# Kernel tuning notes

Hardware: AMD Instinct MI355X
Metric: run time of the kernel (lower is better)

## Reference

```python
import jax, jax.numpy as jnp
import numpy as np

N_NODES = 1_000_000
N_EDGES = 16_000_000
F_IN, F_H1, F_H2, N_CLS = 32, 16, 8, 5
N_GRAPHS = 10_000


def setup_inputs() -> dict:
    key = jax.random.key(0)
    ks = jax.random.split(key, 10)
    x = jax.random.normal(ks[0], (N_NODES, F_IN), dtype=jnp.float32)
    edge_index = jax.random.randint(ks[1], (2, N_EDGES), 0, N_NODES, dtype=jnp.int32)
    batch = jnp.sort(jax.random.randint(ks[2], (N_NODES,), 0, N_GRAPHS, dtype=jnp.int32))
    # learned params (Glorot-ish scale)
    W1 = jax.random.normal(ks[3], (F_IN, F_H1), dtype=jnp.float32) / np.sqrt(F_IN)
    b1 = jnp.zeros((F_H1,), dtype=jnp.float32)
    W2 = jax.random.normal(ks[4], (F_H1, F_H2), dtype=jnp.float32) / np.sqrt(F_H1)
    b2 = jnp.zeros((F_H2,), dtype=jnp.float32)
    Wl = jax.random.normal(ks[5], (F_H2, N_CLS), dtype=jnp.float32) / np.sqrt(F_H2)
    bl = jnp.zeros((N_CLS,), dtype=jnp.float32)
    return {"x": x, "edge_index": edge_index, "batch": batch, "num_graphs": N_GRAPHS,
            "W1": W1, "b1": b1, "W2": W2, "b2": b2, "Wl": Wl, "bl": bl}


def _gcn_conv(x, W, b, src, dst, deg_inv_sqrt, norm_e, num_nodes):
    # h = X W, then symmetric-normalized aggregation with self loops:
    # out_i = sum_{(j->i)} norm_ji * h_j + deg_i^{-1} * h_i + b
    h = x @ W                                  # [N, F_out]
    msg = h[src] * norm_e[:, None]             # [E, F_out] gather + scale
    agg = jax.ops.segment_sum(msg, dst, num_segments=num_nodes)
    self_loop = h * (deg_inv_sqrt * deg_inv_sqrt)[:, None]
    return agg + self_loop + b


def reference(x, edge_index, batch, num_graphs, W1, b1, W2, b2, Wl, bl):
    num_nodes = x.shape[0]
    src, dst = edge_index[0], edge_index[1]
    # degrees including self loops (GCN: A_hat = A + I)
    deg = jax.ops.segment_sum(jnp.ones_like(dst, dtype=x.dtype), dst,
                              num_segments=num_nodes) + 1.0
    deg_inv_sqrt = jax.lax.rsqrt(deg)
    norm_e = deg_inv_sqrt[src] * deg_inv_sqrt[dst]   # [E]

    h = _gcn_conv(x, W1, b1, src, dst, deg_inv_sqrt, norm_e, num_nodes)
    h = jax.nn.relu(h)
    h = _gcn_conv(h, W2, b2, src, dst, deg_inv_sqrt, norm_e, num_nodes)
    h = jax.nn.relu(h)

    # global_mean_pool over graph ids
    sums = jax.ops.segment_sum(h, batch, num_segments=num_graphs)     # [G, F_H2]
    cnts = jax.ops.segment_sum(jnp.ones((num_nodes,), dtype=h.dtype), batch,
                               num_segments=num_graphs)
    pooled = sums / jnp.maximum(cnts, 1.0)[:, None]
    return pooled @ Wl + bl
```

## Files before the change

kernel.cpp:

```cpp
#include <hip/hip_runtime.h>


namespace {

constexpr int F_IN = 32, F_H1 = 16, F_H2 = 8, N_CLS = 5;

__global__ void k_deg(const int* __restrict__ dst, float* __restrict__ deg, int E) {
  int e = blockIdx.x * blockDim.x + threadIdx.x;
  if (e < E) atomicAdd(&deg[dst[e]], 1.0f);
}

__global__ void k_dis(float* __restrict__ d, int N) {
  int i = blockIdx.x * blockDim.x + threadIdx.x;
  if (i < N) d[i] = rsqrtf(d[i] + 1.0f);
}

__global__ void k_mm1(const float* __restrict__ x, const float* __restrict__ W,
                      float* __restrict__ h, int N) {
  __shared__ float w[F_IN * F_H1];
  for (int k = threadIdx.x; k < F_IN * F_H1; k += blockDim.x) w[k] = W[k];
  __syncthreads();
  int i = blockIdx.x * blockDim.x + threadIdx.x;
  if (i >= N) return;
  const float4* xr = reinterpret_cast<const float4*>(x + (size_t)i * F_IN);
  float acc[F_H1];
#pragma unroll
  for (int f = 0; f < F_H1; ++f) acc[f] = 0.f;
#pragma unroll
  for (int k4 = 0; k4 < F_IN / 4; ++k4) {
    float4 v = xr[k4];
    float vv[4] = {v.x, v.y, v.z, v.w};
#pragma unroll
    for (int j = 0; j < 4; ++j) {
      const float* wr = &w[(k4 * 4 + j) * F_H1];
#pragma unroll
      for (int f = 0; f < F_H1; ++f) acc[f] = fmaf(vv[j], wr[f], acc[f]);
    }
  }
  float4* hr = reinterpret_cast<float4*>(h + (size_t)i * F_H1);
#pragma unroll
  for (int q = 0; q < F_H1 / 4; ++q)
    hr[q] = make_float4(acc[q * 4], acc[q * 4 + 1], acc[q * 4 + 2], acc[q * 4 + 3]);
}

__global__ void k_mm2(const float* __restrict__ in, const float* __restrict__ W,
                      float* __restrict__ h, int N) {
  __shared__ float w[F_H1 * F_H2];
  for (int k = threadIdx.x; k < F_H1 * F_H2; k += blockDim.x) w[k] = W[k];
  __syncthreads();
  int i = blockIdx.x * blockDim.x + threadIdx.x;
  if (i >= N) return;
  const float4* xr = reinterpret_cast<const float4*>(in + (size_t)i * F_H1);
  float acc[F_H2];
#pragma unroll
  for (int f = 0; f < F_H2; ++f) acc[f] = 0.f;
#pragma unroll
  for (int k4 = 0; k4 < F_H1 / 4; ++k4) {
    float4 v = xr[k4];
    float vv[4] = {v.x, v.y, v.z, v.w};
#pragma unroll
    for (int j = 0; j < 4; ++j) {
      const float* wr = &w[(k4 * 4 + j) * F_H2];
#pragma unroll
      for (int f = 0; f < F_H2; ++f) acc[f] = fmaf(vv[j], wr[f], acc[f]);
    }
  }
  float4* hr = reinterpret_cast<float4*>(h + (size_t)i * F_H2);
#pragma unroll
  for (int q = 0; q < F_H2 / 4; ++q)
    hr[q] = make_float4(acc[q * 4], acc[q * 4 + 1], acc[q * 4 + 2], acc[q * 4 + 3]);
}

template <int F>
__global__ void k_edge(const int* __restrict__ src, const int* __restrict__ dst,
                       const float* __restrict__ dis, const float* __restrict__ h,
                       float* __restrict__ agg, int total) {
  int gid = blockIdx.x * blockDim.x + threadIdx.x;
  if (gid >= total) return;
  int e = gid / F, f = gid % F;
  int s = src[e], d = dst[e];
  float nw = dis[s] * dis[d];
  atomicAdd(&agg[d * F + f], h[s * F + f] * nw);
}

template <int F>
__global__ void k_combine(const float* __restrict__ h, const float* __restrict__ dis,
                          const float* __restrict__ b, float* __restrict__ agg,
                          int total) {
  int gid = blockIdx.x * blockDim.x + threadIdx.x;
  if (gid >= total) return;
  int i = gid / F, f = gid % F;
  float di = dis[i];
  float v = agg[gid] + h[gid] * di * di + b[f];
  agg[gid] = fmaxf(v, 0.f);
}

__global__ void k_combine_pool(const float* __restrict__ h2, const float* __restrict__ agg2,
                               const float* __restrict__ dis, const float* __restrict__ b,
                               const int* __restrict__ batch, float* __restrict__ pooled,
                               float* __restrict__ cnts, int total) {
  int gid = blockIdx.x * blockDim.x + threadIdx.x;
  if (gid >= total) return;
  int i = gid >> 3, f = gid & 7;
  float di = dis[i];
  float v = fmaxf(agg2[gid] + h2[gid] * di * di + b[f], 0.f);
  int g = batch[i];
  atomicAdd(&pooled[g * F_H2 + f], v);
  if (f == 0) atomicAdd(&cnts[g], 1.0f);
}

__global__ void k_final(const float* __restrict__ pooled, const float* __restrict__ cnts,
                        const float* __restrict__ Wl, const float* __restrict__ bl,
                        float* __restrict__ out, int total) {
  int gid = blockIdx.x * blockDim.x + threadIdx.x;
  if (gid >= total) return;
  int g = gid / N_CLS, c = gid % N_CLS;
  float s = 0.f;
#pragma unroll
  for (int f = 0; f < F_H2; ++f) s += pooled[g * F_H2 + f] * Wl[f * N_CLS + c];
  out[gid] = s / fmaxf(cnts[g], 1.f) + bl[c];
}

}

extern "C" void kernel_launch(void* const* d_in, const int* in_sizes, int n_in,
                              void* d_out, int out_size, void* d_ws, size_t ws_size,
                              hipStream_t stream) {
  const float* x   = (const float*)d_in[0];
  const int* ei    = (const int*)d_in[1];
  const int* batch = (const int*)d_in[2];
  const float* W1 = (const float*)d_in[4];
  const float* b1 = (const float*)d_in[5];
  const float* W2 = (const float*)d_in[6];
  const float* b2 = (const float*)d_in[7];
  const float* Wl = (const float*)d_in[8];
  const float* bl = (const float*)d_in[9];

  const int N = in_sizes[0] / F_IN;
  const int E = in_sizes[1] / 2;
  const int G = out_size / N_CLS;
  const int* src = ei;
  const int* dstp = ei + E;

  float* ws = (float*)d_ws;
  float* dis    = ws;
  float* A      = ws + N;
  float* B      = A + (size_t)N * F_H1;
  float* h2     = A;
  float* agg2   = A + (size_t)N * F_H2;
  float* pooled = B + (size_t)N * F_H1;
  float* cnts   = pooled + (size_t)G * F_H2;

  const int BLK = 256;

  hipMemsetAsync(dis, 0, (size_t)N * sizeof(float), stream);
  hipMemsetAsync(B, 0, (size_t)N * F_H1 * sizeof(float), stream);
  hipMemsetAsync(pooled, 0, ((size_t)G * F_H2 + G) * sizeof(float), stream);

  k_deg<<<(E + BLK - 1) / BLK, BLK, 0, stream>>>(dstp, dis, E);
  k_dis<<<(N + BLK - 1) / BLK, BLK, 0, stream>>>(dis, N);

  k_mm1<<<(N + BLK - 1) / BLK, BLK, 0, stream>>>(x, W1, A, N);
  {
    int total = E * F_H1;
    k_edge<F_H1><<<(unsigned)((long long)(total + BLK - 1) / BLK), BLK, 0, stream>>>(
        src, dstp, dis, A, B, total);
  }
  k_combine<F_H1><<<(N * F_H1 + BLK - 1) / BLK, BLK, 0, stream>>>(A, dis, b1, B, N * F_H1);

  hipMemsetAsync(agg2, 0, (size_t)N * F_H2 * sizeof(float), stream);
  k_mm2<<<(N + BLK - 1) / BLK, BLK, 0, stream>>>(B, W2, h2, N);
  {
    int total = E * F_H2;
    k_edge<F_H2><<<(unsigned)((long long)(total + BLK - 1) / BLK), BLK, 0, stream>>>(
        src, dstp, dis, h2, agg2, total);
  }
  k_combine_pool<<<(N * F_H2 + BLK - 1) / BLK, BLK, 0, stream>>>(
      h2, agg2, dis, b2, batch, pooled, cnts, N * F_H2);

  k_final<<<(G * N_CLS + BLK - 1) / BLK, BLK, 0, stream>>>(
      pooled, cnts, Wl, bl, (float*)d_out, G * N_CLS);
}
```

Before: 3.135 ms.

## Build CSR by destination and replace atomic scatter with pull aggregation

Each call now builds a CSR grouped by destination node: it counts in-degrees, runs a three-stage prefix scan, then scatters source ids into place with atomic cursors. Both GCN layers then use a pull kernel in which each node's threads gather their neighbours' features and fuse the self-loop, bias and ReLU. The second layer also does the mean-pool accumulation in the same kernel. This removes the per-edge-per-feature float atomics and the separate combine kernels, at the cost of an extra integer atomic pass, the scan, an E-sized CSR buffer and unbalanced per-node loops. The old atomic path is kept as a fallback when the workspace is too small.

```diff
diff --git a/kernel.cpp b/kernel.cpp
--- a/kernel.cpp
+++ b/kernel.cpp
@@ -4,16 +4,8 @@
 namespace {
 
 constexpr int F_IN = 32, F_H1 = 16, F_H2 = 8, N_CLS = 5;
-
-__global__ void k_deg(const int* __restrict__ dst, float* __restrict__ deg, int E) {
-  int e = blockIdx.x * blockDim.x + threadIdx.x;
-  if (e < E) atomicAdd(&deg[dst[e]], 1.0f);
-}
-
-__global__ void k_dis(float* __restrict__ d, int N) {
-  int i = blockIdx.x * blockDim.x + threadIdx.x;
-  if (i < N) d[i] = rsqrtf(d[i] + 1.0f);
-}
+constexpr int SCAN_BLK = 256, SCAN_ELEMS = 1024;
+
 
 __global__ void k_mm1(const float* __restrict__ x, const float* __restrict__ W,
                       float* __restrict__ h, int N) {
@@ -71,6 +63,166 @@
     hr[q] = make_float4(acc[q * 4], acc[q * 4 + 1], acc[q * 4 + 2], acc[q * 4 + 3]);
 }
 
+__global__ void k_final(const float* __restrict__ pooled, const float* __restrict__ cnts,
+                        const float* __restrict__ Wl, const float* __restrict__ bl,
+                        float* __restrict__ out, int total) {
+  int gid = blockIdx.x * blockDim.x + threadIdx.x;
+  if (gid >= total) return;
+  int g = gid / N_CLS, c = gid % N_CLS;
+  float s = 0.f;
+#pragma unroll
+  for (int f = 0; f < F_H2; ++f) s += pooled[g * F_H2 + f] * Wl[f * N_CLS + c];
+  out[gid] = s / fmaxf(cnts[g], 1.f) + bl[c];
+}
+
+
+__global__ void k_count(const int* __restrict__ dst, int* __restrict__ cnt, int E) {
+  int e = blockIdx.x * blockDim.x + threadIdx.x;
+  if (e < E) atomicAdd(&cnt[dst[e]], 1);
+}
+
+__global__ void k_scan1(const int* __restrict__ cnt, int* __restrict__ blk, int N) {
+  __shared__ int s[SCAN_BLK];
+  int b = blockIdx.x, t = threadIdx.x;
+  int base = b * SCAN_ELEMS + t * 4;
+  int v = 0;
+#pragma unroll
+  for (int k = 0; k < 4; ++k) {
+    int i = base + k;
+    if (i < N) v += cnt[i];
+  }
+  s[t] = v;
+  __syncthreads();
+  for (int off = SCAN_BLK / 2; off > 0; off >>= 1) {
+    if (t < off) s[t] += s[t + off];
+    __syncthreads();
+  }
+  if (t == 0) blk[b] = s[0];
+}
+
+__global__ void k_scan2(int* __restrict__ blk, int NB, int* __restrict__ row_ptr,
+                        int N, int E) {
+  __shared__ int s[1024];
+  int t = threadIdx.x;
+  int v = (t < NB) ? blk[t] : 0;
+  s[t] = v;
+  __syncthreads();
+  for (int off = 1; off < 1024; off <<= 1) {
+    int x = (t >= off) ? s[t - off] : 0;
+    __syncthreads();
+    s[t] += x;
+    __syncthreads();
+  }
+  if (t < NB) blk[t] = s[t] - v;
+  if (t == 0) row_ptr[N] = E;
+}
+
+__global__ void k_scan3(int* __restrict__ cnt, const int* __restrict__ blk,
+                        int* __restrict__ row_ptr, float* __restrict__ dis, int N) {
+  __shared__ int s[SCAN_BLK];
+  int b = blockIdx.x, t = threadIdx.x;
+  int base = b * SCAN_ELEMS + t * 4;
+  int v[4];
+  int sum = 0;
+#pragma unroll
+  for (int k = 0; k < 4; ++k) {
+    int i = base + k;
+    v[k] = (i < N) ? cnt[i] : 0;
+    sum += v[k];
+  }
+  s[t] = sum;
+  __syncthreads();
+  for (int off = 1; off < SCAN_BLK; off <<= 1) {
+    int x = (t >= off) ? s[t - off] : 0;
+    __syncthreads();
+    s[t] += x;
+    __syncthreads();
+  }
+  int run = blk[b] + s[t] - sum;
+#pragma unroll
+  for (int k = 0; k < 4; ++k) {
+    int i = base + k;
+    if (i < N) {
+      row_ptr[i] = run;
+      cnt[i] = run;
+      dis[i] = rsqrtf((float)v[k] + 1.0f);
+      run += v[k];
+    }
+  }
+}
+
+__global__ void k_scatter(const int* __restrict__ src, const int* __restrict__ dst,
+                          int* __restrict__ cursor, int* __restrict__ csr, int E) {
+  int e = blockIdx.x * blockDim.x + threadIdx.x;
+  if (e >= E) return;
+  int d = dst[e];
+  int pos = atomicAdd(&cursor[d], 1);
+  csr[pos] = src[e];
+}
+
+
+template <int F>
+__global__ void k_pull(const int* __restrict__ row_ptr, const int* __restrict__ csr,
+                       const float* __restrict__ dis, const float* __restrict__ h,
+                       const float* __restrict__ b, float* __restrict__ out, int N) {
+  int t = threadIdx.x;
+  int node = blockIdx.x * (256 / F) + t / F;
+  int f = t % F;
+  if (node >= N) return;
+  int beg = row_ptr[node], end = row_ptr[node + 1];
+  float self = h[(size_t)node * F + f];
+  float acc = 0.f;
+  int e = beg;
+  for (; e + 1 < end; e += 2) {
+    int s0 = csr[e], s1 = csr[e + 1];
+    acc = fmaf(dis[s0], h[(size_t)s0 * F + f], acc);
+    acc = fmaf(dis[s1], h[(size_t)s1 * F + f], acc);
+  }
+  if (e < end) {
+    int s0 = csr[e];
+    acc = fmaf(dis[s0], h[(size_t)s0 * F + f], acc);
+  }
+  float di = dis[node];
+  out[(size_t)node * F + f] = fmaxf(fmaf(di, acc, fmaf(self, di * di, b[f])), 0.f);
+}
+
+__global__ void k_pull_pool(const int* __restrict__ row_ptr, const int* __restrict__ csr,
+                            const float* __restrict__ dis, const float* __restrict__ h,
+                            const float* __restrict__ b, const int* __restrict__ batch,
+                            float* __restrict__ pooled, float* __restrict__ cnts, int N) {
+  int t = threadIdx.x;
+  int node = blockIdx.x * (256 / F_H2) + t / F_H2;
+  int f = t % F_H2;
+  if (node >= N) return;
+  int beg = row_ptr[node], end = row_ptr[node + 1];
+  float self = h[(size_t)node * F_H2 + f];
+  float acc = 0.f;
+  int e = beg;
+  for (; e + 1 < end; e += 2) {
+    int s0 = csr[e], s1 = csr[e + 1];
+    acc = fmaf(dis[s0], h[(size_t)s0 * F_H2 + f], acc);
+    acc = fmaf(dis[s1], h[(size_t)s1 * F_H2 + f], acc);
+  }
+  if (e < end) {
+    int s0 = csr[e];
+    acc = fmaf(dis[s0], h[(size_t)s0 * F_H2 + f], acc);
+  }
+  float di = dis[node];
+  float v = fmaxf(fmaf(di, acc, fmaf(self, di * di, b[f])), 0.f);
+  int g = batch[node];
+  atomicAdd(&pooled[g * F_H2 + f], v);
+  if (f == 0) atomicAdd(&cnts[g], 1.0f);
+}
+
+
+__global__ void k_deg(const int* __restrict__ dst, float* __restrict__ deg, int E) {
+  int e = blockIdx.x * blockDim.x + threadIdx.x;
+  if (e < E) atomicAdd(&deg[dst[e]], 1.0f);
+}
+__global__ void k_dis(float* __restrict__ d, int N) {
+  int i = blockIdx.x * blockDim.x + threadIdx.x;
+  if (i < N) d[i] = rsqrtf(d[i] + 1.0f);
+}
 template <int F>
 __global__ void k_edge(const int* __restrict__ src, const int* __restrict__ dst,
                        const float* __restrict__ dis, const float* __restrict__ h,
@@ -79,22 +231,17 @@
   if (gid >= total) return;
   int e = gid / F, f = gid % F;
   int s = src[e], d = dst[e];
-  float nw = dis[s] * dis[d];
-  atomicAdd(&agg[d * F + f], h[s * F + f] * nw);
-}
-
+  atomicAdd(&agg[d * F + f], h[s * F + f] * dis[s] * dis[d]);
+}
 template <int F>
 __global__ void k_combine(const float* __restrict__ h, const float* __restrict__ dis,
-                          const float* __restrict__ b, float* __restrict__ agg,
-                          int total) {
+                          const float* __restrict__ b, float* __restrict__ agg, int total) {
   int gid = blockIdx.x * blockDim.x + threadIdx.x;
   if (gid >= total) return;
   int i = gid / F, f = gid % F;
   float di = dis[i];
-  float v = agg[gid] + h[gid] * di * di + b[f];
-  agg[gid] = fmaxf(v, 0.f);
-}
-
+  agg[gid] = fmaxf(agg[gid] + h[gid] * di * di + b[f], 0.f);
+}
 __global__ void k_combine_pool(const float* __restrict__ h2, const float* __restrict__ agg2,
                                const float* __restrict__ dis, const float* __restrict__ b,
                                const int* __restrict__ batch, float* __restrict__ pooled,
@@ -109,18 +256,6 @@
   if (f == 0) atomicAdd(&cnts[g], 1.0f);
 }
 
-__global__ void k_final(const float* __restrict__ pooled, const float* __restrict__ cnts,
-                        const float* __restrict__ Wl, const float* __restrict__ bl,
-                        float* __restrict__ out, int total) {
-  int gid = blockIdx.x * blockDim.x + threadIdx.x;
-  if (gid >= total) return;
-  int g = gid / N_CLS, c = gid % N_CLS;
-  float s = 0.f;
-#pragma unroll
-  for (int f = 0; f < F_H2; ++f) s += pooled[g * F_H2 + f] * Wl[f * N_CLS + c];
-  out[gid] = s / fmaxf(cnts[g], 1.f) + bl[c];
-}
-
 }
 
 extern "C" void kernel_launch(void* const* d_in, const int* in_sizes, int n_in,
@@ -139,8 +274,53 @@
   const int N = in_sizes[0] / F_IN;
   const int E = in_sizes[1] / 2;
   const int G = out_size / N_CLS;
-  const int* src = ei;
+  const int* src  = ei;
   const int* dstp = ei + E;
+
+  const int BLK = 256;
+  const int NB = (N + SCAN_ELEMS - 1) / SCAN_ELEMS;
+
+  size_t need = (size_t)N * 4
+              + (size_t)(N + 4) * 4
+              + (size_t)N * 4
+              + (size_t)E * 4
+              + (size_t)N * F_H1 * 4
+              + (size_t)N * F_H1 * 4
+              + (size_t)G * F_H2 * 4 + (size_t)G * 4 + 4096 * 4;
+
+  if (ws_size >= need) {
+    char* p = (char*)d_ws;
+    int*   cnt     = (int*)p;    p += (size_t)N * 4;
+    int*   row_ptr = (int*)p;    p += (size_t)(N + 4) * 4;
+    float* dis     = (float*)p;  p += (size_t)N * 4;
+    int*   csr     = (int*)p;    p += (size_t)E * 4;
+    float* H       = (float*)p;  p += (size_t)N * F_H1 * 4;
+    float* O       = (float*)p;  p += (size_t)N * F_H1 * 4;
+    float* pooled  = (float*)p;  p += (size_t)G * F_H2 * 4;
+    float* cnts    = (float*)p;  p += (size_t)G * 4;
+    int*   blk     = (int*)p;
+    float* h2 = H;
+
+    hipMemsetAsync(cnt, 0, (size_t)N * 4, stream);
+    hipMemsetAsync(pooled, 0, ((size_t)G * F_H2 + G) * 4, stream);
+
+    k_count<<<(E + BLK - 1) / BLK, BLK, 0, stream>>>(dstp, cnt, E);
+    k_scan1<<<NB, SCAN_BLK, 0, stream>>>(cnt, blk, N);
+    k_scan2<<<1, 1024, 0, stream>>>(blk, NB, row_ptr, N, E);
+    k_scan3<<<NB, SCAN_BLK, 0, stream>>>(cnt, blk, row_ptr, dis, N);
+    k_scatter<<<(E + BLK - 1) / BLK, BLK, 0, stream>>>(src, dstp, cnt, csr, E);
+
+    k_mm1<<<(N + BLK - 1) / BLK, BLK, 0, stream>>>(x, W1, H, N);
+    k_pull<F_H1><<<(N * F_H1 + BLK - 1) / BLK, BLK, 0, stream>>>(
+        row_ptr, csr, dis, H, b1, O, N);
+    k_mm2<<<(N + BLK - 1) / BLK, BLK, 0, stream>>>(O, W2, h2, N);
+    k_pull_pool<<<(N * F_H2 + BLK - 1) / BLK, BLK, 0, stream>>>(
+        row_ptr, csr, dis, h2, b2, batch, pooled, cnts, N);
+
+    k_final<<<(G * N_CLS + BLK - 1) / BLK, BLK, 0, stream>>>(
+        pooled, cnts, Wl, bl, (float*)d_out, G * N_CLS);
+    return;
+  }
 
   float* ws = (float*)d_ws;
   float* dis    = ws;
@@ -151,33 +331,20 @@
   float* pooled = B + (size_t)N * F_H1;
   float* cnts   = pooled + (size_t)G * F_H2;
 
-  const int BLK = 256;
-
   hipMemsetAsync(dis, 0, (size_t)N * sizeof(float), stream);
   hipMemsetAsync(B, 0, (size_t)N * F_H1 * sizeof(float), stream);
   hipMemsetAsync(pooled, 0, ((size_t)G * F_H2 + G) * sizeof(float), stream);
 
   k_deg<<<(E + BLK - 1) / BLK, BLK, 0, stream>>>(dstp, dis, E);
   k_dis<<<(N + BLK - 1) / BLK, BLK, 0, stream>>>(dis, N);
-
   k_mm1<<<(N + BLK - 1) / BLK, BLK, 0, stream>>>(x, W1, A, N);
-  {
-    int total = E * F_H1;
-    k_edge<F_H1><<<(unsigned)((long long)(total + BLK - 1) / BLK), BLK, 0, stream>>>(
-        src, dstp, dis, A, B, total);
-  }
+  k_edge<F_H1><<<(E * F_H1 + BLK - 1) / BLK, BLK, 0, stream>>>(src, dstp, dis, A, B, E * F_H1);
   k_combine<F_H1><<<(N * F_H1 + BLK - 1) / BLK, BLK, 0, stream>>>(A, dis, b1, B, N * F_H1);
-
   hipMemsetAsync(agg2, 0, (size_t)N * F_H2 * sizeof(float), stream);
   k_mm2<<<(N + BLK - 1) / BLK, BLK, 0, stream>>>(B, W2, h2, N);
-  {
-    int total = E * F_H2;
-    k_edge<F_H2><<<(unsigned)((long long)(total + BLK - 1) / BLK), BLK, 0, stream>>>(
-        src, dstp, dis, h2, agg2, total);
-  }
+  k_edge<F_H2><<<(E * F_H2 + BLK - 1) / BLK, BLK, 0, stream>>>(src, dstp, dis, h2, agg2, E * F_H2);
   k_combine_pool<<<(N * F_H2 + BLK - 1) / BLK, BLK, 0, stream>>>(
       h2, agg2, dis, b2, batch, pooled, cnts, N * F_H2);
-
   k_final<<<(G * N_CLS + BLK - 1) / BLK, BLK, 0, stream>>>(
       pooled, cnts, Wl, bl, (float*)d_out, G * N_CLS);
 }
```

Result: no change. 3.159 ms (+0.8%).

## Bucket edges by destination block and aggregate in shared memory

Applied to the files above, without the earlier changes.

Adds a counting-sort preprocessing step that bins edges into 1024-node destination buckets and packs the local destination with the source index into one int. Degree counting and both GCN aggregations then run one block per bucket, accumulating in LDS instead of global atomics, with the self-loop, bias, ReLU and pooling fused into the epilogue. This removes tens of millions of contended global float atomics at the cost of an extra histogram, scan and scatter pass over the edges, and it depends on the workspace being large enough. The old atomic path stays as a fallback.

```diff
diff --git a/kernel.cpp b/kernel.cpp
--- a/kernel.cpp
+++ b/kernel.cpp
@@ -4,16 +4,10 @@
 namespace {
 
 constexpr int F_IN = 32, F_H1 = 16, F_H2 = 8, N_CLS = 5;
-
-__global__ void k_deg(const int* __restrict__ dst, float* __restrict__ deg, int E) {
-  int e = blockIdx.x * blockDim.x + threadIdx.x;
-  if (e < E) atomicAdd(&deg[dst[e]], 1.0f);
-}
-
-__global__ void k_dis(float* __restrict__ d, int N) {
-  int i = blockIdx.x * blockDim.x + threadIdx.x;
-  if (i < N) d[i] = rsqrtf(d[i] + 1.0f);
-}
+constexpr int BB = 10, NPB = 1 << BB;
+constexpr int MAXB = 1024;
+constexpr int CHUNK = 12288;
+
 
 __global__ void k_mm1(const float* __restrict__ x, const float* __restrict__ W,
                       float* __restrict__ h, int N) {
@@ -71,6 +65,215 @@
     hr[q] = make_float4(acc[q * 4], acc[q * 4 + 1], acc[q * 4 + 2], acc[q * 4 + 3]);
 }
 
+__global__ void k_final(const float* __restrict__ pooled, const float* __restrict__ cnts,
+                        const float* __restrict__ Wl, const float* __restrict__ bl,
+                        float* __restrict__ out, int total) {
+  int gid = blockIdx.x * blockDim.x + threadIdx.x;
+  if (gid >= total) return;
+  int g = gid / N_CLS, c = gid % N_CLS;
+  float s = 0.f;
+#pragma unroll
+  for (int f = 0; f < F_H2; ++f) s += pooled[g * F_H2 + f] * Wl[f * N_CLS + c];
+  out[gid] = s / fmaxf(cnts[g], 1.f) + bl[c];
+}
+
+
+__global__ void k_hist(const int* __restrict__ dst, int* __restrict__ bcnt,
+                       int E, int nbuck) {
+  __shared__ int h[MAXB];
+  for (int i = threadIdx.x; i < MAXB; i += blockDim.x) h[i] = 0;
+  __syncthreads();
+  for (int e = blockIdx.x * blockDim.x + threadIdx.x; e < E;
+       e += gridDim.x * blockDim.x)
+    atomicAdd(&h[dst[e] >> BB], 1);
+  __syncthreads();
+  for (int i = threadIdx.x; i < nbuck; i += blockDim.x)
+    if (h[i]) atomicAdd(&bcnt[i], h[i]);
+}
+
+__global__ void k_bscan(const int* __restrict__ bcnt, int* __restrict__ bbase,
+                        int* __restrict__ bcur, int nbuck, int E) {
+  __shared__ int s[MAXB];
+  int t = threadIdx.x;
+  int v = (t < nbuck) ? bcnt[t] : 0;
+  s[t] = v;
+  __syncthreads();
+  for (int off = 1; off < MAXB; off <<= 1) {
+    int x = (t >= off) ? s[t - off] : 0;
+    __syncthreads();
+    s[t] += x;
+    __syncthreads();
+  }
+  int ex = s[t] - v;
+  if (t < nbuck) { bbase[t] = ex; bcur[t] = ex; }
+  if (t == 0) bbase[nbuck] = E;
+}
+
+__global__ __launch_bounds__(256)
+void k_binscatter(const int* __restrict__ dst, const int* __restrict__ src,
+                  int* __restrict__ bcur, int* __restrict__ packed, int E) {
+  __shared__ int hist[MAXB];
+  __shared__ int sbase[MAXB];
+  __shared__ int lcur[MAXB];
+  __shared__ int stg[CHUNK];
+  __shared__ int stmp[256];
+  int t = threadIdx.x;
+  int c0 = blockIdx.x * CHUNK;
+  int n = min(CHUNK, E - c0);
+  for (int i = t; i < MAXB; i += 256) hist[i] = 0;
+  __syncthreads();
+  for (int j = t; j < n; j += 256) atomicAdd(&hist[dst[c0 + j] >> BB], 1);
+  __syncthreads();
+  int v[4], sum = 0;
+  int b4 = t * 4;
+#pragma unroll
+  for (int k = 0; k < 4; ++k) { v[k] = hist[b4 + k]; sum += v[k]; }
+  stmp[t] = sum;
+  __syncthreads();
+  for (int off = 1; off < 256; off <<= 1) {
+    int x = (t >= off) ? stmp[t - off] : 0;
+    __syncthreads();
+    stmp[t] += x;
+    __syncthreads();
+  }
+  int run = stmp[t] - sum;
+#pragma unroll
+  for (int k = 0; k < 4; ++k) { sbase[b4 + k] = run; lcur[b4 + k] = run; run += v[k]; }
+  __syncthreads();
+  for (int i = t; i < MAXB; i += 256) {
+    int c = hist[i];
+    if (c) hist[i] = atomicAdd(&bcur[i], c);
+  }
+  __syncthreads();
+  for (int j = t; j < n; j += 256) {
+    int d = dst[c0 + j], s = src[c0 + j];
+    int b = d >> BB;
+    int p = atomicAdd(&lcur[b], 1);
+    stg[p] = ((d & (NPB - 1)) << 20) | s;
+  }
+  __syncthreads();
+  for (int j = t; j < n; j += 256) {
+    int lo = 0, hi = MAXB - 1;
+    while (lo < hi) {
+      int mid = (lo + hi + 1) >> 1;
+      if (sbase[mid] <= j) lo = mid; else hi = mid - 1;
+    }
+    packed[hist[lo] + (j - sbase[lo])] = stg[j];
+  }
+}
+
+__global__ void k_dis_b(const int* __restrict__ bbase, const int* __restrict__ packed,
+                        float* __restrict__ dis, int N) {
+  __shared__ int cnt[NPB];
+  int t = threadIdx.x;
+  for (int i = t; i < NPB; i += blockDim.x) cnt[i] = 0;
+  __syncthreads();
+  int b = blockIdx.x;
+  int beg = bbase[b], end = bbase[b + 1];
+  for (int e = beg + t; e < end; e += blockDim.x)
+    atomicAdd(&cnt[packed[e] >> 20], 1);
+  __syncthreads();
+  int node0 = b << BB;
+  for (int i = t; i < NPB; i += blockDim.x) {
+    int node = node0 + i;
+    if (node < N) dis[node] = rsqrtf((float)cnt[i] + 1.0f);
+  }
+}
+
+
+template <int F>
+__global__ __launch_bounds__(512)
+void k_conv(const int* __restrict__ bbase, const int* __restrict__ packed,
+            const float* __restrict__ dis, const float* __restrict__ h,
+            const float* __restrict__ bias, float* __restrict__ out, int N) {
+  __shared__ float acc[NPB * F];
+  int t = threadIdx.x;
+  for (int i = t; i < NPB * F; i += 512) acc[i] = 0.f;
+  __syncthreads();
+  int b = blockIdx.x;
+  int beg = bbase[b], end = bbase[b + 1];
+  const int EPI = 512 / F;
+  int f = t % F, eg = t / F;
+  for (int e = beg + eg; e < end; e += 2 * EPI) {
+    int p0 = packed[e];
+    int s0 = p0 & ((1 << 20) - 1), d0 = p0 >> 20;
+    float m0 = dis[s0] * h[(size_t)s0 * F + f];
+    int e1 = e + EPI;
+    if (e1 < end) {
+      int p1 = packed[e1];
+      int s1 = p1 & ((1 << 20) - 1), d1 = p1 >> 20;
+      float m1 = dis[s1] * h[(size_t)s1 * F + f];
+      atomicAdd(&acc[d0 * F + f], m0);
+      atomicAdd(&acc[d1 * F + f], m1);
+    } else {
+      atomicAdd(&acc[d0 * F + f], m0);
+    }
+  }
+  __syncthreads();
+  int node0 = b << BB;
+  for (int i = t; i < NPB * F; i += 512) {
+    int node = node0 + i / F;
+    if (node >= N) continue;
+    int ff = i % F;
+    float di = dis[node];
+    float v = fmaf(di, acc[i], fmaf(di * di, h[(size_t)node * F + ff], bias[ff]));
+    out[(size_t)node * F + ff] = fmaxf(v, 0.f);
+  }
+}
+
+__global__ __launch_bounds__(512)
+void k_conv_pool(const int* __restrict__ bbase, const int* __restrict__ packed,
+                 const float* __restrict__ dis, const float* __restrict__ h,
+                 const float* __restrict__ bias, const int* __restrict__ batch,
+                 float* __restrict__ pooled, float* __restrict__ cnts, int N) {
+  constexpr int F = F_H2;
+  __shared__ float acc[NPB * F];
+  int t = threadIdx.x;
+  for (int i = t; i < NPB * F; i += 512) acc[i] = 0.f;
+  __syncthreads();
+  int b = blockIdx.x;
+  int beg = bbase[b], end = bbase[b + 1];
+  const int EPI = 512 / F;
+  int f = t % F, eg = t / F;
+  for (int e = beg + eg; e < end; e += 2 * EPI) {
+    int p0 = packed[e];
+    int s0 = p0 & ((1 << 20) - 1), d0 = p0 >> 20;
+    float m0 = dis[s0] * h[(size_t)s0 * F + f];
+    int e1 = e + EPI;
+    if (e1 < end) {
+      int p1 = packed[e1];
+      int s1 = p1 & ((1 << 20) - 1), d1 = p1 >> 20;
+      float m1 = dis[s1] * h[(size_t)s1 * F + f];
+      atomicAdd(&acc[d0 * F + f], m0);
+      atomicAdd(&acc[d1 * F + f], m1);
+    } else {
+      atomicAdd(&acc[d0 * F + f], m0);
+    }
+  }
+  __syncthreads();
+  int node0 = b << BB;
+  for (int i = t; i < NPB * F; i += 512) {
+    int node = node0 + i / F;
+    if (node >= N) continue;
+    int ff = i % F;
+    float di = dis[node];
+    float v = fmaf(di, acc[i], fmaf(di * di, h[(size_t)node * F + ff], bias[ff]));
+    v = fmaxf(v, 0.f);
+    int g = batch[node];
+    atomicAdd(&pooled[g * F_H2 + ff], v);
+    if (ff == 0) atomicAdd(&cnts[g], 1.0f);
+  }
+}
+
+
+__global__ void k_deg(const int* __restrict__ dst, float* __restrict__ deg, int E) {
+  int e = blockIdx.x * blockDim.x + threadIdx.x;
+  if (e < E) atomicAdd(&deg[dst[e]], 1.0f);
+}
+__global__ void k_dis(float* __restrict__ d, int N) {
+  int i = blockIdx.x * blockDim.x + threadIdx.x;
+  if (i < N) d[i] = rsqrtf(d[i] + 1.0f);
+}
 template <int F>
 __global__ void k_edge(const int* __restrict__ src, const int* __restrict__ dst,
                        const float* __restrict__ dis, const float* __restrict__ h,
@@ -79,26 +282,21 @@
   if (gid >= total) return;
   int e = gid / F, f = gid % F;
   int s = src[e], d = dst[e];
-  float nw = dis[s] * dis[d];
-  atomicAdd(&agg[d * F + f], h[s * F + f] * nw);
-}
-
+  atomicAdd(&agg[d * F + f], h[s * F + f] * dis[s] * dis[d]);
+}
 template <int F>
 __global__ void k_combine(const float* __restrict__ h, const float* __restrict__ dis,
-                          const float* __restrict__ b, float* __restrict__ agg,
-                          int total) {
+                          const float* __restrict__ b, float* __restrict__ agg, int total) {
   int gid = blockIdx.x * blockDim.x + threadIdx.x;
   if (gid >= total) return;
   int i = gid / F, f = gid % F;
   float di = dis[i];
-  float v = agg[gid] + h[gid] * di * di + b[f];
-  agg[gid] = fmaxf(v, 0.f);
-}
-
-__global__ void k_combine_pool(const float* __restrict__ h2, const float* __restrict__ agg2,
-                               const float* __restrict__ dis, const float* __restrict__ b,
-                               const int* __restrict__ batch, float* __restrict__ pooled,
-                               float* __restrict__ cnts, int total) {
+  agg[gid] = fmaxf(agg[gid] + h[gid] * di * di + b[f], 0.f);
+}
+__global__ void k_combine_pool_fb(const float* __restrict__ h2, const float* __restrict__ agg2,
+                                  const float* __restrict__ dis, const float* __restrict__ b,
+                                  const int* __restrict__ batch, float* __restrict__ pooled,
+                                  float* __restrict__ cnts, int total) {
   int gid = blockIdx.x * blockDim.x + threadIdx.x;
   if (gid >= total) return;
   int i = gid >> 3, f = gid & 7;
@@ -107,18 +305,6 @@
   int g = batch[i];
   atomicAdd(&pooled[g * F_H2 + f], v);
   if (f == 0) atomicAdd(&cnts[g], 1.0f);
-}
-
-__global__ void k_final(const float* __restrict__ pooled, const float* __restrict__ cnts,
-                        const float* __restrict__ Wl, const float* __restrict__ bl,
-                        float* __restrict__ out, int total) {
-  int gid = blockIdx.x * blockDim.x + threadIdx.x;
-  if (gid >= total) return;
-  int g = gid / N_CLS, c = gid % N_CLS;
-  float s = 0.f;
-#pragma unroll
-  for (int f = 0; f < F_H2; ++f) s += pooled[g * F_H2 + f] * Wl[f * N_CLS + c];
-  out[gid] = s / fmaxf(cnts[g], 1.f) + bl[c];
 }
 
 }
@@ -139,8 +325,49 @@
   const int N = in_sizes[0] / F_IN;
   const int E = in_sizes[1] / 2;
   const int G = out_size / N_CLS;
-  const int* src = ei;
+  const int* src  = ei;
   const int* dstp = ei + E;
+
+  const int BLK = 256;
+  const int nbuck = (N + NPB - 1) >> BB;
+
+  size_t need = (size_t)(3 * MAXB + 8) * 4
+              + (size_t)E * 4
+              + (size_t)N * 4
+              + (size_t)N * F_H1 * 4
+              + (size_t)N * F_H1 * 4
+              + (size_t)G * (F_H2 + 1) * 4 + 1024;
+
+  if (N <= (1 << 20) && nbuck <= MAXB && ws_size >= need) {
+    char* p = (char*)d_ws;
+    int*   bcnt   = (int*)p;    p += (size_t)MAXB * 4;
+    int*   bbase  = (int*)p;    p += (size_t)(MAXB + 4) * 4;
+    int*   bcur   = (int*)p;    p += (size_t)MAXB * 4;
+    int*   packed = (int*)p;    p += (size_t)E * 4;
+    float* dis    = (float*)p;  p += (size_t)N * 4;
+    float* H      = (float*)p;  p += (size_t)N * F_H1 * 4;
+    float* O      = (float*)p;  p += (size_t)N * F_H1 * 4;
+    float* pooled = (float*)p;  p += (size_t)G * F_H2 * 4;
+    float* cnts   = (float*)p;
+
+    hipMemsetAsync(bcnt, 0, (size_t)MAXB * 4, stream);
+    hipMemsetAsync(pooled, 0, ((size_t)G * F_H2 + G) * 4, stream);
+
+    k_hist<<<2048, BLK, 0, stream>>>(dstp, bcnt, E, nbuck);
+    k_bscan<<<1, MAXB, 0, stream>>>(bcnt, bbase, bcur, nbuck, E);
+    k_binscatter<<<(E + CHUNK - 1) / CHUNK, BLK, 0, stream>>>(dstp, src, bcur, packed, E);
+    k_dis_b<<<nbuck, BLK, 0, stream>>>(bbase, packed, dis, N);
+
+    k_mm1<<<(N + BLK - 1) / BLK, BLK, 0, stream>>>(x, W1, H, N);
+    k_conv<F_H1><<<nbuck, 512, 0, stream>>>(bbase, packed, dis, H, b1, O, N);
+    k_mm2<<<(N + BLK - 1) / BLK, BLK, 0, stream>>>(O, W2, H, N);
+    k_conv_pool<<<nbuck, 512, 0, stream>>>(bbase, packed, dis, H, b2, batch,
+                                           pooled, cnts, N);
+
+    k_final<<<(G * N_CLS + BLK - 1) / BLK, BLK, 0, stream>>>(
+        pooled, cnts, Wl, bl, (float*)d_out, G * N_CLS);
+    return;
+  }
 
   float* ws = (float*)d_ws;
   float* dis    = ws;
@@ -151,33 +378,20 @@
   float* pooled = B + (size_t)N * F_H1;
   float* cnts   = pooled + (size_t)G * F_H2;
 
-  const int BLK = 256;
-
   hipMemsetAsync(dis, 0, (size_t)N * sizeof(float), stream);
   hipMemsetAsync(B, 0, (size_t)N * F_H1 * sizeof(float), stream);
   hipMemsetAsync(pooled, 0, ((size_t)G * F_H2 + G) * sizeof(float), stream);
 
   k_deg<<<(E + BLK - 1) / BLK, BLK, 0, stream>>>(dstp, dis, E);
   k_dis<<<(N + BLK - 1) / BLK, BLK, 0, stream>>>(dis, N);
-
   k_mm1<<<(N + BLK - 1) / BLK, BLK, 0, stream>>>(x, W1, A, N);
-  {
-    int total = E * F_H1;
-    k_edge<F_H1><<<(unsigned)((long long)(total + BLK - 1) / BLK), BLK, 0, stream>>>(
-        src, dstp, dis, A, B, total);
-  }
+  k_edge<F_H1><<<(E * F_H1 + BLK - 1) / BLK, BLK, 0, stream>>>(src, dstp, dis, A, B, E * F_H1);
   k_combine<F_H1><<<(N * F_H1 + BLK - 1) / BLK, BLK, 0, stream>>>(A, dis, b1, B, N * F_H1);
-
   hipMemsetAsync(agg2, 0, (size_t)N * F_H2 * sizeof(float), stream);
   k_mm2<<<(N + BLK - 1) / BLK, BLK, 0, stream>>>(B, W2, h2, N);
-  {
-    int total = E * F_H2;
-    k_edge<F_H2><<<(unsigned)((long long)(total + BLK - 1) / BLK), BLK, 0, stream>>>(
-        src, dstp, dis, h2, agg2, total);
-  }
-  k_combine_pool<<<(N * F_H2 + BLK - 1) / BLK, BLK, 0, stream>>>(
+  k_edge<F_H2><<<(E * F_H2 + BLK - 1) / BLK, BLK, 0, stream>>>(src, dstp, dis, h2, agg2, E * F_H2);
+  k_combine_pool_fb<<<(N * F_H2 + BLK - 1) / BLK, BLK, 0, stream>>>(
       h2, agg2, dis, b2, batch, pooled, cnts, N * F_H2);
-
   k_final<<<(G * N_CLS + BLK - 1) / BLK, BLK, 0, stream>>>(
       pooled, cnts, Wl, bl, (float*)d_out, G * N_CLS);
 }
```

After: 2.881 ms. 1.09x faster.
